# Kernel optimization log

Measured on AMD Instinct MI355X. Metric: run time of the kernel, lower is better.

The kernel has to match this reference:

```python
import jax, jax.numpy as jnp
import numpy as np

N = 50000      # nodes
E = 800000     # edges
P = 3          # pos_dim
F = 64         # feats_dim
M = 32         # m_dim
L = 2          # n_layers
EIN = 2 * F + 1  # edge_input_dim = 129
EPS = 1e-8


def _xavier(key, shape):
    # per-layer stacked xavier-normal weights, shape = (in, out)
    fan_in, fan_out = shape
    std = (2.0 / (fan_in + fan_out)) ** 0.5
    return std * jax.random.normal(key, (L,) + shape, jnp.float32)


def setup_inputs() -> dict:
    key = jax.random.key(0)
    ks = jax.random.split(key, 10)
    x = jax.random.normal(ks[0], (N, P + F), jnp.float32)
    edge_index = jax.random.randint(ks[1], (2, E), 0, N)
    return {
        "x": x,
        "edge_index": edge_index,
        # edge_mlp: Linear(EIN, 2*EIN) -> SiLU -> Linear(2*EIN, M) -> SiLU
        "eW1": _xavier(ks[2], (EIN, 2 * EIN)), "eb1": jnp.zeros((L, 2 * EIN), jnp.float32),
        "eW2": _xavier(ks[3], (2 * EIN, M)),   "eb2": jnp.zeros((L, M), jnp.float32),
        # coors_mlp: Linear(M, 4*M) -> SiLU -> Linear(4*M, 1) -> Tanh
        "cW1": _xavier(ks[4], (M, 4 * M)),     "cb1": jnp.zeros((L, 4 * M), jnp.float32),
        "cW2": _xavier(ks[5], (4 * M, 1)),     "cb2": jnp.zeros((L, 1), jnp.float32),
        # node_mlp: Linear(F+M, 2*F) -> SiLU -> Linear(2*F, F)
        "nW1": _xavier(ks[6], (F + M, 2 * F)), "nb1": jnp.zeros((L, 2 * F), jnp.float32),
        "nW2": _xavier(ks[7], (2 * F, F)),     "nb2": jnp.zeros((L, F), jnp.float32),
        # CoorsNorm learned scale (init 0.01) per layer
        "cscale": jnp.full((L, 1), 0.01, jnp.float32),
    }


def reference(x, edge_index, eW1, eb1, eW2, eb2, cW1, cb1, cW2, cb2,
              nW1, nb1, nW2, nb2, cscale):
    src = edge_index[0]  # x_j (source)
    dst = edge_index[1]  # x_i (target / aggregation index)
    for l in range(L):
        coors, feats = x[:, :P], x[:, P:]
        rel = coors[src] - coors[dst]                       # (E, 3)
        rel_dist = jnp.sum(rel * rel, axis=-1, keepdims=True)  # (E, 1)
        # per-edge message MLP
        e_in = jnp.concatenate([feats[dst], feats[src], rel_dist], axis=-1)  # (E, 129)
        h = jax.nn.silu(e_in @ eW1[l] + eb1[l])             # (E, 258)
        m_ij = jax.nn.silu(h @ eW2[l] + eb2[l])             # (E, 32)
        # coordinate weights: SiLU MLP -> tanh
        cw = jnp.tanh(jax.nn.silu(m_ij @ cW1[l] + cb1[l]) @ cW2[l] + cb2[l])  # (E, 1)
        # CoorsNorm on rel_coors
        norm = jnp.linalg.norm(rel, axis=-1, keepdims=True)
        rel_n = rel / jnp.maximum(norm, EPS) * cscale[l]
        # scatter-aggregate (aggr='add')
        mhat_i = jax.ops.segment_sum(cw * rel_n, dst, num_segments=N)  # (N, 3)
        coors_out = coors + mhat_i
        m_i = jax.ops.segment_sum(m_ij, dst, num_segments=N)           # (N, 32)
        # node update MLP with residual
        n_in = jnp.concatenate([feats, m_i], axis=-1)                  # (N, 96)
        upd = jax.nn.silu(n_in @ nW1[l] + nb1[l]) @ nW2[l] + nb2[l]    # (N, 64)
        x = jnp.concatenate([coors_out, feats + upd], axis=-1)
    return x
```

## Files before the change

kernel.cpp:

```cpp
#include <hip/hip_runtime.h>

#define N_NODES 50000
#define N_EDGES 800000
#define PDIM 3
#define FDIM 64
#define MDIM 32
#define NLAYERS 2
#define EINDIM 129
#define H1 258
#define CH 128
#define NH 128
#define XDIM 67
#define K1P 136
#define H1T 288
#define HSTR 168
#define W1T_K 136
#define MLSTR 40
#define NINS 104
#define NH1S 136
#define NW2K 128

typedef __attribute__((ext_vector_type(8))) short short8;
typedef __attribute__((ext_vector_type(4))) float f32x4;

#define LOG2E 1.4426950408889634f

__device__ __forceinline__ float fsilu(float x) {
  float e = __builtin_amdgcn_exp2f(-x * LOG2E);
  return x * __builtin_amdgcn_rcpf(1.0f + e);
}

__device__ __forceinline__ float ftanh(float x) {
  float xc = fminf(fmaxf(x, -15.0f), 15.0f);
  float E = __builtin_amdgcn_exp2f(2.0f * LOG2E * xc);
  return (E - 1.0f) * __builtin_amdgcn_rcpf(E + 1.0f);
}

__device__ __forceinline__ unsigned short f2bf(float f) {
  union { float f; unsigned u; } v; v.f = f;
  unsigned r = v.u + 0x7FFF + ((v.u >> 16) & 1);
  return (unsigned short)(r >> 16);
}

__device__ __forceinline__ unsigned cvt_pk(float lo, float hi) {
  unsigned r;
  asm("v_cvt_pk_bf16_f32 %0, %1, %2" : "=v"(r) : "v"(lo), "v"(hi));
  return r;
}

__device__ __forceinline__ int xcd_swz(int bid, int nwg) {
  const int nx = 8;
  int q = nwg / nx, r = nwg % nx;
  int xcd = bid % nx, idx = bid / nx;
  return (xcd < r) ? xcd * (q + 1) + idx : r * (q + 1) + (xcd - r) * q + idx;
}

__global__ void count_kernel(const int* __restrict__ ei, int* __restrict__ cnt) {
  int e = blockIdx.x * 256 + threadIdx.x;
  if (e < N_EDGES) atomicAdd(&cnt[ei[N_EDGES + e]], 1);
}

__global__ __launch_bounds__(1024)
void scan_kernel(const int* __restrict__ cnt, int* __restrict__ csr, int* __restrict__ cursor) {
  __shared__ int partial[1024];
  const int tid = threadIdx.x;
  const int CHUNK = 49;
  int base = tid * CHUNK;
  int s = 0;
  for (int i = 0; i < CHUNK; ++i) {
    int idx = base + i;
    if (idx < N_NODES) s += cnt[idx];
  }
  partial[tid] = s;
  __syncthreads();
  for (int off = 1; off < 1024; off <<= 1) {
    int v = (tid >= off) ? partial[tid - off] : 0;
    __syncthreads();
    partial[tid] += v;
    __syncthreads();
  }
  int run = partial[tid] - s;
  for (int i = 0; i < CHUNK; ++i) {
    int idx = base + i;
    if (idx < N_NODES) {
      csr[idx] = run;
      cursor[idx] = run;
      run += cnt[idx];
    }
  }
  if (tid == 1023) csr[N_NODES] = run;
}

__global__ void rank_kernel(const int* __restrict__ ei, int* __restrict__ cursor,
                            int* __restrict__ srcS, int* __restrict__ dstS) {
  int e = blockIdx.x * 256 + threadIdx.x;
  if (e < N_EDGES) {
    int s = ei[e];
    int d = ei[N_EDGES + e];
    int p = atomicAdd(&cursor[d], 1);
    srcS[p] = s;
    dstS[p] = d;
  }
}

__global__ void prep_weights(const float* __restrict__ eW1, const float* __restrict__ eW2,
                             const float* __restrict__ cW1, const float* __restrict__ eb1,
                             const float* __restrict__ nW1, const float* __restrict__ nW2,
                             unsigned short* __restrict__ w1t, unsigned short* __restrict__ w2t,
                             unsigned short* __restrict__ cw1t,
                             unsigned short* __restrict__ nw1t, unsigned short* __restrict__ nw2t,
                             float* __restrict__ b1p, float* __restrict__ wrp) {
  int idx = blockIdx.x * 256 + threadIdx.x;
  const int n1 = NLAYERS * H1T * W1T_K;
  const int n2 = NLAYERS * MDIM * H1T;
  const int n3 = NLAYERS * CH * MDIM;
  const int n4 = NLAYERS * H1T;
  const int n5 = NLAYERS * NH * NINS;
  const int n6 = NLAYERS * FDIM * NW2K;
  if (idx < n1) {
    int k = idx % W1T_K;
    int rest = idx / W1T_K;
    int j = rest % H1T;
    int l = rest / H1T;
    float v = (k < 128 && j < H1) ? eW1[(l * EINDIM + k) * H1 + j] : 0.0f;
    w1t[idx] = f2bf(v);
  } else if (idx < n1 + n2) {
    int t = idx - n1;
    int k = t % H1T;
    int rest = t / H1T;
    int n = rest % MDIM;
    int l = rest / MDIM;
    float v = (k < H1) ? eW2[(l * H1 + k) * MDIM + n] : 0.0f;
    w2t[t] = f2bf(v);
  } else if (idx < n1 + n2 + n3) {
    int t = idx - n1 - n2;
    int k = t % MDIM;
    int rest = t / MDIM;
    int n = rest % CH;
    int l = rest / CH;
    cw1t[t] = f2bf(cW1[(l * MDIM + k) * CH + n]);
  } else if (idx < n1 + n2 + n3 + n4) {
    int t = idx - n1 - n2 - n3;
    int j = t % H1T;
    int l = t / H1T;
    b1p[t] = (j < H1) ? eb1[l * H1 + j] : 0.0f;
  } else if (idx < n1 + n2 + n3 + 2 * n4) {
    int t = idx - n1 - n2 - n3 - n4;
    int j = t % H1T;
    int l = t / H1T;
    wrp[t] = (j < H1) ? eW1[((size_t)l * EINDIM + 128) * H1 + j] : 0.0f;
  } else if (idx < n1 + n2 + n3 + 2 * n4 + n5) {
    int t = idx - n1 - n2 - n3 - 2 * n4;
    int k = t % NINS;
    int rest = t / NINS;
    int j = rest % NH;
    int l = rest / NH;
    float v = (k < FDIM + MDIM) ? nW1[(l * (FDIM + MDIM) + k) * NH + j] : 0.0f;
    nw1t[t] = f2bf(v);
  } else if (idx < n1 + n2 + n3 + 2 * n4 + n5 + n6) {
    int t = idx - n1 - n2 - n3 - 2 * n4 - n5;
    int k = t % NW2K;
    int rest = t / NW2K;
    int j = rest % FDIM;
    int l = rest / FDIM;
    nw2t[t] = f2bf(nW2[(l * NH + k) * FDIM + j]);
  }
}

__global__ void convert_x(const float* __restrict__ X, unsigned short* __restrict__ Xb) {
  int idx = blockIdx.x * 256 + threadIdx.x;
  if (idx >= N_NODES * 8) return;
  int n = idx >> 3, c = idx & 7;
  const float* src = X + n * XDIM + PDIM + c * 8;
  short8 v;
  #pragma unroll
  for (int i = 0; i < 8; ++i) v[i] = (short)f2bf(src[i]);
  *(short8*)&Xb[n * 64 + c * 8] = v;
}

__global__ __launch_bounds__(256, 3)
void edge_mfma_kernel(const float* __restrict__ X,
                      const unsigned short* __restrict__ Xb,
                      const int* __restrict__ srcS, const int* __restrict__ dstS,
                      const unsigned short* __restrict__ w1t,
                      const float* __restrict__ b1p, const float* __restrict__ wrp,
                      const unsigned short* __restrict__ w2t, const float* __restrict__ eb2,
                      const unsigned short* __restrict__ cw1t, const float* __restrict__ cb1,
                      const float* __restrict__ cW2, const float* __restrict__ cb2,
                      const float* __restrict__ cscale,
                      unsigned short* __restrict__ ms, float* __restrict__ mh4,
                      int layer)
{
  __shared__ unsigned short einLds[64 * K1P];
  __shared__ unsigned short hLds[64 * HSTR];
  __shared__ unsigned short ml[64 * MLSTR];
  __shared__ float distLds[64];
  __shared__ float rel3[64 * 3];
  __shared__ int sdS[64], sdD[64];

  const int tid = threadIdx.x;
  const int lane = tid & 63;
  const int wid = tid >> 6;
  const int ln15 = lane & 15;
  const int kg = lane >> 4;
  const int e0 = xcd_swz(blockIdx.x, gridDim.x) * 64;
  const int erow = wid * 16 + ln15;

  if (tid < 64) {
    int s = srcS[e0 + tid];
    int d = dstS[e0 + tid];
    sdS[tid] = s; sdD[tid] = d;
    float rx = X[s * XDIM + 0] - X[d * XDIM + 0];
    float ry = X[s * XDIM + 1] - X[d * XDIM + 1];
    float rz = X[s * XDIM + 2] - X[d * XDIM + 2];
    rel3[tid * 3 + 0] = rx;
    rel3[tid * 3 + 1] = ry;
    rel3[tid * 3 + 2] = rz;
    distLds[tid] = rx * rx + ry * ry + rz * rz;
  }
  __syncthreads();

  #pragma unroll
  for (int it = 0; it < 4; ++it) {
    int idx = tid + it * 256;
    int e = idx >> 4, c = idx & 15;
    int node = (c < 8) ? sdD[e] : sdS[e];
    short8 v = *(const short8*)&Xb[node * 64 + (c & 7) * 8];
    *(short8*)&einLds[e * K1P + c * 8] = v;
  }
  __syncthreads();

  float distE[4];
  #pragma unroll
  for (int et = 0; et < 4; ++et) distE[et] = distLds[et * 16 + ln15];

  const unsigned short* W1T = w1t + layer * H1T * W1T_K;
  const float* B1P = b1p + layer * H1T;
  const float* WRP = wrp + layer * H1T;
  const unsigned short* W2T = w2t + layer * MDIM * H1T;
  const float* B2 = eb2 + layer * MDIM;

  float b20 = B2[ln15], b21 = B2[16 + ln15];
  f32x4 mac0 = {b20, b20, b20, b20};
  f32x4 mac1 = {b21, b21, b21, b21};

  #pragma unroll 1
  for (int half = 0; half < 2; ++half) {
    const int jt0 = half ? 10 : 0;
    const int njt = half ? 8 : 10;
    for (int jl = wid; jl < njt; jl += 4) {
      const int jt = jt0 + jl;
      f32x4 b4 = *(const f32x4*)&B1P[jt * 16 + kg * 4];
      f32x4 w4 = *(const f32x4*)&WRP[jt * 16 + kg * 4];
      short8 a[4];
      #pragma unroll
      for (int ks = 0; ks < 4; ++ks)
        a[ks] = *(const short8*)&W1T[(jt * 16 + ln15) * W1T_K + ks * 32 + kg * 8];
      #pragma unroll
      for (int et = 0; et < 4; ++et) {
        f32x4 acc;
        #pragma unroll
        for (int r = 0; r < 4; ++r) acc[r] = fmaf(distE[et], w4[r], b4[r]);
        #pragma unroll
        for (int ks = 0; ks < 4; ++ks) {
          short8 b = *(const short8*)&einLds[(et * 16 + ln15) * K1P + ks * 32 + kg * 8];
          acc = __builtin_amdgcn_mfma_f32_16x16x32_bf16(a[ks], b, acc, 0, 0, 0);
        }
        uint2 uu;
        uu.x = cvt_pk(fsilu(acc[0]), fsilu(acc[1]));
        uu.y = cvt_pk(fsilu(acc[2]), fsilu(acc[3]));
        *(uint2*)&hLds[(et * 16 + ln15) * HSTR + jl * 16 + kg * 4] = uu;
      }
    }
    __syncthreads();

    const int nks = half ? 4 : 5;
    #pragma unroll
    for (int ksl = 0; ksl < nks; ++ksl) {
      const int kglob = half * 160 + ksl * 32;
      short8 ah = *(const short8*)&hLds[erow * HSTR + ksl * 32 + kg * 8];
      short8 w0 = *(const short8*)&W2T[ln15 * H1T + kglob + kg * 8];
      short8 w1 = *(const short8*)&W2T[(16 + ln15) * H1T + kglob + kg * 8];
      mac0 = __builtin_amdgcn_mfma_f32_16x16x32_bf16(ah, w0, mac0, 0, 0, 0);
      mac1 = __builtin_amdgcn_mfma_f32_16x16x32_bf16(ah, w1, mac1, 0, 0, 0);
    }
    if (half == 0) __syncthreads();
  }

  #pragma unroll
  for (int r = 0; r < 4; ++r) {
    int e = wid * 16 + kg * 4 + r;
    ml[e * MLSTR + ln15] = f2bf(fsilu(mac0[r]));
    ml[e * MLSTR + 16 + ln15] = f2bf(fsilu(mac1[r]));
  }

  const unsigned short* CW1T = cw1t + layer * CH * MDIM;
  const float* CB1 = cb1 + layer * CH;
  const float* CW2v = cW2 + layer * CH;
  short8 am = *(const short8*)&ml[erow * MLSTR + kg * 8];
  float psum[4] = {0.f, 0.f, 0.f, 0.f};
  #pragma unroll
  for (int nt = 0; nt < 8; ++nt) {
    float cb = CB1[nt * 16 + ln15];
    f32x4 cacc = {cb, cb, cb, cb};
    short8 bc = *(const short8*)&CW1T[(nt * 16 + ln15) * MDIM + kg * 8];
    cacc = __builtin_amdgcn_mfma_f32_16x16x32_bf16(am, bc, cacc, 0, 0, 0);
    float w2v = CW2v[nt * 16 + ln15];
    #pragma unroll
    for (int r = 0; r < 4; ++r) psum[r] += fsilu(cacc[r]) * w2v;
  }
  #pragma unroll
  for (int off = 1; off < 16; off <<= 1) {
    #pragma unroll
    for (int r = 0; r < 4; ++r) psum[r] += __shfl_xor(psum[r], off, 64);
  }
  float cwv = 0.0f;
  #pragma unroll
  for (int r = 0; r < 4; ++r) {
    float t = __shfl(psum[r], ((lane & 15) >> 2) * 16, 64);
    if ((lane & 3) == r) cwv = t;
  }

  {
    int e_loc = lane >> 2, seg = lane & 3;
    short8 v = *(const short8*)&ml[(wid * 16 + e_loc) * MLSTR + seg * 8];
    *(short8*)&ms[(size_t)(e0 + wid * 16 + e_loc) * MDIM + seg * 8] = v;
  }
  if (lane < 16) {
    int eg = e0 + erow;
    float cw = ftanh(cwv + cb2[layer]);
    float fac = cw * cscale[layer] / fmaxf(sqrtf(distLds[erow]), 1e-8f);
    *(float4*)&mh4[(size_t)eg * 4] =
        make_float4(fac * rel3[erow * 3 + 0], fac * rel3[erow * 3 + 1],
                    fac * rel3[erow * 3 + 2], 0.0f);
  }
}

__global__ __launch_bounds__(256, 3)
void node_mfma_kernel(const float* __restrict__ Xin,
                      const unsigned short* __restrict__ XbIn,
                      const unsigned short* __restrict__ ms,
                      const float* __restrict__ mh4,
                      const int* __restrict__ csr,
                      const unsigned short* __restrict__ nw1t, const float* __restrict__ nb1,
                      const unsigned short* __restrict__ nw2t, const float* __restrict__ nb2,
                      float* __restrict__ Xout, unsigned short* __restrict__ XbOut,
                      int writeXb, int layer)
{
  __shared__ unsigned short ninLds[64 * NINS];
  __shared__ unsigned short h1Lds[64 * NH1S];
  __shared__ float outLds[64 * 68];
  __shared__ float mhsLds[64][3];
  __shared__ int csrLds[65];

  const int tid = threadIdx.x;
  const int lane = tid & 63;
  const int wid = tid >> 6;
  const int ln15 = lane & 15;
  const int kg = lane >> 4;
  const int n0 = xcd_swz(blockIdx.x, gridDim.x) * 64;

  if (tid < 65) {
    int nn = n0 + tid;
    csrLds[tid] = (nn <= N_NODES) ? csr[nn] : 0;
  }
  #pragma unroll
  for (int it = 0; it < 2; ++it) {
    int idx = tid + it * 256;
    int nl = idx >> 3, c = idx & 7;
    int n = n0 + nl;
    uint4 v = make_uint4(0, 0, 0, 0);
    if (n < N_NODES) v = *(const uint4*)&XbIn[n * 64 + c * 8];
    *(uint4*)&ninLds[nl * NINS + c * 8] = v;
  }
  __syncthreads();

  {
    const int nl = tid >> 2, sub = tid & 3;
    const int n = n0 + nl;
    int off = csrLds[nl], end = csrLds[nl + 1];
    if (n >= N_NODES) { off = 0; end = 0; }
    float s0 = 0, s1 = 0, s2 = 0, s3 = 0, s4 = 0, s5 = 0, s6 = 0, s7 = 0;
    for (int r = off; r < end; ++r) {
      uint4 q = *(const uint4*)&ms[(size_t)r * MDIM + sub * 8];
      union { unsigned u; float f; } t;
      t.u = q.x << 16;         s0 += t.f;
      t.u = q.x & 0xFFFF0000u; s1 += t.f;
      t.u = q.y << 16;         s2 += t.f;
      t.u = q.y & 0xFFFF0000u; s3 += t.f;
      t.u = q.z << 16;         s4 += t.f;
      t.u = q.z & 0xFFFF0000u; s5 += t.f;
      t.u = q.w << 16;         s6 += t.f;
      t.u = q.w & 0xFFFF0000u; s7 += t.f;
    }
    uint4 mo;
    mo.x = cvt_pk(s0, s1);
    mo.y = cvt_pk(s2, s3);
    mo.z = cvt_pk(s4, s5);
    mo.w = cvt_pk(s6, s7);
    *(uint4*)&ninLds[nl * NINS + FDIM + sub * 8] = mo;

    float mx = 0, my = 0, mz = 0;
    for (int r = off + sub; r < end; r += 4) {
      float4 q = *(const float4*)&mh4[(size_t)r * 4];
      mx += q.x; my += q.y; mz += q.z;
    }
    mx += __shfl_xor(mx, 1, 64); mx += __shfl_xor(mx, 2, 64);
    my += __shfl_xor(my, 1, 64); my += __shfl_xor(my, 2, 64);
    mz += __shfl_xor(mz, 1, 64); mz += __shfl_xor(mz, 2, 64);
    if (sub == 0) {
      mhsLds[nl][0] = mx; mhsLds[nl][1] = my; mhsLds[nl][2] = mz;
    }
  }
  __syncthreads();

  const unsigned short* W1 = nw1t + layer * NH * NINS;
  const float* B1 = nb1 + layer * NH;
  for (int jt = wid; jt < 8; jt += 4) {
    f32x4 b4 = *(const f32x4*)&B1[jt * 16 + kg * 4];
    short8 a[3];
    #pragma unroll
    for (int ks = 0; ks < 3; ++ks)
      a[ks] = *(const short8*)&W1[(jt * 16 + ln15) * NINS + ks * 32 + kg * 8];
    #pragma unroll
    for (int et = 0; et < 4; ++et) {
      f32x4 acc = b4;
      #pragma unroll
      for (int ks = 0; ks < 3; ++ks) {
        short8 b = *(const short8*)&ninLds[(et * 16 + ln15) * NINS + ks * 32 + kg * 8];
        acc = __builtin_amdgcn_mfma_f32_16x16x32_bf16(a[ks], b, acc, 0, 0, 0);
      }
      uint2 uu;
      uu.x = cvt_pk(fsilu(acc[0]), fsilu(acc[1]));
      uu.y = cvt_pk(fsilu(acc[2]), fsilu(acc[3]));
      *(uint2*)&h1Lds[(et * 16 + ln15) * NH1S + jt * 16 + kg * 4] = uu;
    }
  }
  __syncthreads();

  const unsigned short* W2 = nw2t + layer * FDIM * NW2K;
  const float* B2 = nb2 + layer * FDIM;
  {
    int jt = wid;
    f32x4 b4 = *(const f32x4*)&B2[jt * 16 + kg * 4];
    short8 a[4];
    #pragma unroll
    for (int ks = 0; ks < 4; ++ks)
      a[ks] = *(const short8*)&W2[(jt * 16 + ln15) * NW2K + ks * 32 + kg * 8];
    #pragma unroll
    for (int et = 0; et < 4; ++et) {
      f32x4 acc = b4;
      #pragma unroll
      for (int ks = 0; ks < 4; ++ks) {
        short8 b = *(const short8*)&h1Lds[(et * 16 + ln15) * NH1S + ks * 32 + kg * 8];
        acc = __builtin_amdgcn_mfma_f32_16x16x32_bf16(a[ks], b, acc, 0, 0, 0);
      }
      *(f32x4*)&outLds[(et * 16 + ln15) * 68 + jt * 16 + kg * 4] = acc;
    }
  }
  __syncthreads();

  #pragma unroll
  for (int it = 0; it < 16; ++it) {
    int idx = tid + it * 256;
    int nl = idx >> 6, c = idx & 63;
    int n = n0 + nl;
    if (n < N_NODES) {
      float v = Xin[n * XDIM + PDIM + c] + outLds[nl * 68 + c];
      Xout[n * XDIM + PDIM + c] = v;
      if (writeXb) XbOut[n * 64 + c] = f2bf(v);
    }
  }
  if (tid < 64) {
    int n = n0 + tid;
    if (n < N_NODES) {
      Xout[n * XDIM + 0] = Xin[n * XDIM + 0] + mhsLds[tid][0];
      Xout[n * XDIM + 1] = Xin[n * XDIM + 1] + mhsLds[tid][1];
      Xout[n * XDIM + 2] = Xin[n * XDIM + 2] + mhsLds[tid][2];
    }
  }
}

extern "C" void kernel_launch(void* const* d_in, const int* in_sizes, int n_in,
                              void* d_out, int out_size, void* d_ws, size_t ws_size,
                              hipStream_t stream) {
  const float* x      = (const float*)d_in[0];
  const int*   ei     = (const int*)d_in[1];
  const float* eW1    = (const float*)d_in[2];
  const float* eb1    = (const float*)d_in[3];
  const float* eW2    = (const float*)d_in[4];
  const float* eb2    = (const float*)d_in[5];
  const float* cW1    = (const float*)d_in[6];
  const float* cb1    = (const float*)d_in[7];
  const float* cW2    = (const float*)d_in[8];
  const float* cb2    = (const float*)d_in[9];
  const float* nW1    = (const float*)d_in[10];
  const float* nb1    = (const float*)d_in[11];
  const float* nW2    = (const float*)d_in[12];
  const float* nb2    = (const float*)d_in[13];
  const float* cscale = (const float*)d_in[14];

  float* ws     = (float*)d_ws;
  float* X1     = ws;
  float* mh4    = X1 + N_NODES * XDIM;
  int*   csr    = (int*)(mh4 + (size_t)N_EDGES * 4);
  int*   cursor = csr + N_NODES + 4;
  int*   cnt    = cursor + N_NODES;
  int*   srcS   = cnt + N_NODES;
  int*   dstS   = srcS + N_EDGES;
  unsigned short* w1t  = (unsigned short*)(dstS + N_EDGES);
  unsigned short* w2t  = w1t + NLAYERS * H1T * W1T_K;
  unsigned short* cw1t = w2t + NLAYERS * MDIM * H1T;
  unsigned short* nw1t = cw1t + NLAYERS * CH * MDIM;
  unsigned short* nw2t = nw1t + NLAYERS * NH * NINS;
  float* b1p = (float*)(nw2t + NLAYERS * FDIM * NW2K);
  float* wrp = b1p + NLAYERS * H1T;
  unsigned short* Xb = (unsigned short*)(wrp + NLAYERS * H1T);
  unsigned short* ms = Xb + (size_t)N_NODES * 64;

  hipMemsetAsync(cnt, 0, N_NODES * sizeof(int), stream);
  count_kernel<<<(N_EDGES + 255) / 256, 256, 0, stream>>>(ei, cnt);
  scan_kernel<<<1, 1024, 0, stream>>>(cnt, csr, cursor);
  rank_kernel<<<(N_EDGES + 255) / 256, 256, 0, stream>>>(ei, cursor, srcS, dstS);
  {
    const int total = NLAYERS * (H1T * W1T_K + MDIM * H1T + CH * MDIM + 2 * H1T
                                 + NH * NINS + FDIM * NW2K);
    prep_weights<<<(total + 255) / 256, 256, 0, stream>>>(
        eW1, eW2, cW1, eb1, nW1, nW2, w1t, w2t, cw1t, nw1t, nw2t, b1p, wrp);
  }
  convert_x<<<(N_NODES * 8 + 255) / 256, 256, 0, stream>>>(x, Xb);

  const int nodeBlocks = (N_NODES + 63) / 64;
  for (int l = 0; l < NLAYERS; ++l) {
    const float* Xin = (l == 0) ? x : X1;
    float* Xout = (l == 0) ? X1 : (float*)d_out;
    edge_mfma_kernel<<<N_EDGES / 64, 256, 0, stream>>>(
        Xin, Xb, srcS, dstS, w1t, b1p, wrp, w2t, eb2, cw1t, cb1, cW2, cb2, cscale,
        ms, mh4, l);
    node_mfma_kernel<<<nodeBlocks, 256, 0, stream>>>(
        Xin, Xb, ms, mh4, csr, nw1t, nb1, nw2t, nb2, Xout, Xb, (l == 0) ? 1 : 0, l);
  }
}
```

Measured before the change: 734.9 us.

## Make edge MLP wave-private: per-wave 32-edge tiles with register-held inputs

Each wave now owns 32 edges and computes all hidden tiles for them. Its gathered feature operands stay in registers instead of being staged through a shared einLds buffer, so the block-wide barriers go away. The first layer is processed in three chunks of 96 hidden units, each feeding the second layer immediately. That shrinks the shared h buffer and allows 4 blocks per CU with 128 edges per block. The trade-offs are that every wave loads all W1 tiles itself rather than splitting them across waves, and register pressure goes up.

```diff
diff --git a/kernel.cpp b/kernel.cpp
--- a/kernel.cpp
+++ b/kernel.cpp
@@ -11,9 +11,8 @@
 #define CH 128
 #define NH 128
 #define XDIM 67
-#define K1P 136
 #define H1T 288
-#define HSTR 168
+#define HSTR3 104
 #define W1T_K 136
 #define MLSTR 40
 #define NINS 104
@@ -178,7 +177,7 @@
   *(short8*)&Xb[n * 64 + c * 8] = v;
 }
 
-__global__ __launch_bounds__(256, 3)
+__global__ __launch_bounds__(256, 4)
 void edge_mfma_kernel(const float* __restrict__ X,
                       const unsigned short* __restrict__ Xb,
                       const int* __restrict__ srcS, const int* __restrict__ dstS,
@@ -191,48 +190,38 @@
                       unsigned short* __restrict__ ms, float* __restrict__ mh4,
                       int layer)
 {
-  __shared__ unsigned short einLds[64 * K1P];
-  __shared__ unsigned short hLds[64 * HSTR];
-  __shared__ unsigned short ml[64 * MLSTR];
-  __shared__ float distLds[64];
-  __shared__ float rel3[64 * 3];
-  __shared__ int sdS[64], sdD[64];
+  __shared__ unsigned short hLds[128 * HSTR3];
+  __shared__ unsigned short ml[128 * MLSTR];
 
   const int tid = threadIdx.x;
   const int lane = tid & 63;
   const int wid = tid >> 6;
   const int ln15 = lane & 15;
   const int kg = lane >> 4;
-  const int e0 = xcd_swz(blockIdx.x, gridDim.x) * 64;
-  const int erow = wid * 16 + ln15;
-
-  if (tid < 64) {
-    int s = srcS[e0 + tid];
-    int d = dstS[e0 + tid];
-    sdS[tid] = s; sdD[tid] = d;
-    float rx = X[s * XDIM + 0] - X[d * XDIM + 0];
-    float ry = X[s * XDIM + 1] - X[d * XDIM + 1];
-    float rz = X[s * XDIM + 2] - X[d * XDIM + 2];
-    rel3[tid * 3 + 0] = rx;
-    rel3[tid * 3 + 1] = ry;
-    rel3[tid * 3 + 2] = rz;
-    distLds[tid] = rx * rx + ry * ry + rz * rz;
-  }
-  __syncthreads();
-
-  #pragma unroll
-  for (int it = 0; it < 4; ++it) {
-    int idx = tid + it * 256;
-    int e = idx >> 4, c = idx & 15;
-    int node = (c < 8) ? sdD[e] : sdS[e];
-    short8 v = *(const short8*)&Xb[node * 64 + (c & 7) * 8];
-    *(short8*)&einLds[e * K1P + c * 8] = v;
-  }
-  __syncthreads();
-
-  float distE[4];
-  #pragma unroll
-  for (int et = 0; et < 4; ++et) distE[et] = distLds[et * 16 + ln15];
+  const int e0 = xcd_swz(blockIdx.x, gridDim.x) * 128;
+  const int ew0 = e0 + wid * 32;
+
+  const int eA = ew0 + ln15;
+  const int eB = ew0 + 16 + ln15;
+  const int sA = srcS[eA], dA = dstS[eA];
+  const int sB = srcS[eB], dB = dstS[eB];
+  float rxA = X[sA * XDIM + 0] - X[dA * XDIM + 0];
+  float ryA = X[sA * XDIM + 1] - X[dA * XDIM + 1];
+  float rzA = X[sA * XDIM + 2] - X[dA * XDIM + 2];
+  float rxB = X[sB * XDIM + 0] - X[dB * XDIM + 0];
+  float ryB = X[sB * XDIM + 1] - X[dB * XDIM + 1];
+  float rzB = X[sB * XDIM + 2] - X[dB * XDIM + 2];
+  const float distA = rxA * rxA + ryA * ryA + rzA * rzA;
+  const float distB = rxB * rxB + ryB * ryB + rzB * rzB;
+
+  short8 einB[2][4];
+  #pragma unroll
+  for (int ks = 0; ks < 4; ++ks) {
+    int nA = (ks < 2) ? dA : sA;
+    int nB = (ks < 2) ? dB : sB;
+    einB[0][ks] = *(const short8*)&Xb[nA * 64 + (ks & 1) * 32 + kg * 8];
+    einB[1][ks] = *(const short8*)&Xb[nB * 64 + (ks & 1) * 32 + kg * 8];
+  }
 
   const unsigned short* W1T = w1t + layer * H1T * W1T_K;
   const float* B1P = b1p + layer * H1T;
@@ -241,14 +230,18 @@
   const float* B2 = eb2 + layer * MDIM;
 
   float b20 = B2[ln15], b21 = B2[16 + ln15];
-  f32x4 mac0 = {b20, b20, b20, b20};
-  f32x4 mac1 = {b21, b21, b21, b21};
+  f32x4 mac[2][2];
+  #pragma unroll
+  for (int et = 0; et < 2; ++et) {
+    mac[et][0] = (f32x4){b20, b20, b20, b20};
+    mac[et][1] = (f32x4){b21, b21, b21, b21};
+  }
 
   #pragma unroll 1
-  for (int half = 0; half < 2; ++half) {
-    const int jt0 = half ? 10 : 0;
-    const int njt = half ? 8 : 10;
-    for (int jl = wid; jl < njt; jl += 4) {
+  for (int chunk = 0; chunk < 3; ++chunk) {
+    const int jt0 = chunk * 6;
+    #pragma unroll 2
+    for (int jl = 0; jl < 6; ++jl) {
       const int jt = jt0 + jl;
       f32x4 b4 = *(const f32x4*)&B1P[jt * 16 + kg * 4];
       f32x4 w4 = *(const f32x4*)&WRP[jt * 16 + kg * 4];
@@ -257,82 +250,97 @@
       for (int ks = 0; ks < 4; ++ks)
         a[ks] = *(const short8*)&W1T[(jt * 16 + ln15) * W1T_K + ks * 32 + kg * 8];
       #pragma unroll
-      for (int et = 0; et < 4; ++et) {
+      for (int et = 0; et < 2; ++et) {
+        const float dv = et ? distB : distA;
         f32x4 acc;
         #pragma unroll
-        for (int r = 0; r < 4; ++r) acc[r] = fmaf(distE[et], w4[r], b4[r]);
+        for (int r = 0; r < 4; ++r) acc[r] = fmaf(dv, w4[r], b4[r]);
         #pragma unroll
-        for (int ks = 0; ks < 4; ++ks) {
-          short8 b = *(const short8*)&einLds[(et * 16 + ln15) * K1P + ks * 32 + kg * 8];
-          acc = __builtin_amdgcn_mfma_f32_16x16x32_bf16(a[ks], b, acc, 0, 0, 0);
-        }
+        for (int ks = 0; ks < 4; ++ks)
+          acc = __builtin_amdgcn_mfma_f32_16x16x32_bf16(a[ks], einB[et][ks], acc, 0, 0, 0);
         uint2 uu;
         uu.x = cvt_pk(fsilu(acc[0]), fsilu(acc[1]));
         uu.y = cvt_pk(fsilu(acc[2]), fsilu(acc[3]));
-        *(uint2*)&hLds[(et * 16 + ln15) * HSTR + jl * 16 + kg * 4] = uu;
+        *(uint2*)&hLds[(wid * 32 + et * 16 + ln15) * HSTR3 + jl * 16 + kg * 4] = uu;
       }
     }
-    __syncthreads();
-
-    const int nks = half ? 4 : 5;
-    #pragma unroll
-    for (int ksl = 0; ksl < nks; ++ksl) {
-      const int kglob = half * 160 + ksl * 32;
-      short8 ah = *(const short8*)&hLds[erow * HSTR + ksl * 32 + kg * 8];
+    #pragma unroll
+    for (int ksl = 0; ksl < 3; ++ksl) {
+      const int kglob = chunk * 96 + ksl * 32;
       short8 w0 = *(const short8*)&W2T[ln15 * H1T + kglob + kg * 8];
       short8 w1 = *(const short8*)&W2T[(16 + ln15) * H1T + kglob + kg * 8];
-      mac0 = __builtin_amdgcn_mfma_f32_16x16x32_bf16(ah, w0, mac0, 0, 0, 0);
-      mac1 = __builtin_amdgcn_mfma_f32_16x16x32_bf16(ah, w1, mac1, 0, 0, 0);
-    }
-    if (half == 0) __syncthreads();
-  }
-
-  #pragma unroll
-  for (int r = 0; r < 4; ++r) {
-    int e = wid * 16 + kg * 4 + r;
-    ml[e * MLSTR + ln15] = f2bf(fsilu(mac0[r]));
-    ml[e * MLSTR + 16 + ln15] = f2bf(fsilu(mac1[r]));
+      #pragma unroll
+      for (int et = 0; et < 2; ++et) {
+        short8 ah = *(const short8*)&hLds[(wid * 32 + et * 16 + ln15) * HSTR3 + ksl * 32 + kg * 8];
+        mac[et][0] = __builtin_amdgcn_mfma_f32_16x16x32_bf16(ah, w0, mac[et][0], 0, 0, 0);
+        mac[et][1] = __builtin_amdgcn_mfma_f32_16x16x32_bf16(ah, w1, mac[et][1], 0, 0, 0);
+      }
+    }
+  }
+
+  #pragma unroll
+  for (int et = 0; et < 2; ++et) {
+    #pragma unroll
+    for (int r = 0; r < 4; ++r) {
+      int eg = wid * 32 + et * 16 + kg * 4 + r;
+      ml[eg * MLSTR + ln15] = f2bf(fsilu(mac[et][0][r]));
+      ml[eg * MLSTR + 16 + ln15] = f2bf(fsilu(mac[et][1][r]));
+    }
   }
 
   const unsigned short* CW1T = cw1t + layer * CH * MDIM;
   const float* CB1 = cb1 + layer * CH;
   const float* CW2v = cW2 + layer * CH;
-  short8 am = *(const short8*)&ml[erow * MLSTR + kg * 8];
-  float psum[4] = {0.f, 0.f, 0.f, 0.f};
+  short8 amA = *(const short8*)&ml[(wid * 32 + ln15) * MLSTR + kg * 8];
+  short8 amB = *(const short8*)&ml[(wid * 32 + 16 + ln15) * MLSTR + kg * 8];
+  float psA[4] = {0.f, 0.f, 0.f, 0.f};
+  float psB[4] = {0.f, 0.f, 0.f, 0.f};
   #pragma unroll
   for (int nt = 0; nt < 8; ++nt) {
     float cb = CB1[nt * 16 + ln15];
-    f32x4 cacc = {cb, cb, cb, cb};
+    float w2v = CW2v[nt * 16 + ln15];
     short8 bc = *(const short8*)&CW1T[(nt * 16 + ln15) * MDIM + kg * 8];
-    cacc = __builtin_amdgcn_mfma_f32_16x16x32_bf16(am, bc, cacc, 0, 0, 0);
-    float w2v = CW2v[nt * 16 + ln15];
-    #pragma unroll
-    for (int r = 0; r < 4; ++r) psum[r] += fsilu(cacc[r]) * w2v;
+    f32x4 cA = {cb, cb, cb, cb};
+    f32x4 cB = {cb, cb, cb, cb};
+    cA = __builtin_amdgcn_mfma_f32_16x16x32_bf16(amA, bc, cA, 0, 0, 0);
+    cB = __builtin_amdgcn_mfma_f32_16x16x32_bf16(amB, bc, cB, 0, 0, 0);
+    #pragma unroll
+    for (int r = 0; r < 4; ++r) {
+      psA[r] += fsilu(cA[r]) * w2v;
+      psB[r] += fsilu(cB[r]) * w2v;
+    }
   }
   #pragma unroll
   for (int off = 1; off < 16; off <<= 1) {
     #pragma unroll
-    for (int r = 0; r < 4; ++r) psum[r] += __shfl_xor(psum[r], off, 64);
-  }
-  float cwv = 0.0f;
+    for (int r = 0; r < 4; ++r) {
+      psA[r] += __shfl_xor(psA[r], off, 64);
+      psB[r] += __shfl_xor(psB[r], off, 64);
+    }
+  }
+  float cwvA = 0.0f, cwvB = 0.0f;
   #pragma unroll
   for (int r = 0; r < 4; ++r) {
-    float t = __shfl(psum[r], ((lane & 15) >> 2) * 16, 64);
-    if ((lane & 3) == r) cwv = t;
-  }
-
-  {
-    int e_loc = lane >> 2, seg = lane & 3;
-    short8 v = *(const short8*)&ml[(wid * 16 + e_loc) * MLSTR + seg * 8];
-    *(short8*)&ms[(size_t)(e0 + wid * 16 + e_loc) * MDIM + seg * 8] = v;
-  }
-  if (lane < 16) {
-    int eg = e0 + erow;
+    float tA = __shfl(psA[r], ((lane & 15) >> 2) * 16, 64);
+    float tB = __shfl(psB[r], ((lane & 15) >> 2) * 16, 64);
+    if ((lane & 3) == r) { cwvA = tA; cwvB = tB; }
+  }
+
+  #pragma unroll
+  for (int it = 0; it < 2; ++it) {
+    int idx = lane + it * 64;
+    int el = idx >> 2, seg = idx & 3;
+    short8 v = *(const short8*)&ml[(wid * 32 + el) * MLSTR + seg * 8];
+    *(short8*)&ms[(size_t)(ew0 + el) * MDIM + seg * 8] = v;
+  }
+  if (lane < 32) {
+    const int hi = lane >> 4;
+    float cwv = hi ? cwvB : cwvA;
+    float dv = hi ? distB : distA;
+    float rx = hi ? rxB : rxA, ry = hi ? ryB : ryA, rz = hi ? rzB : rzA;
     float cw = ftanh(cwv + cb2[layer]);
-    float fac = cw * cscale[layer] / fmaxf(sqrtf(distLds[erow]), 1e-8f);
-    *(float4*)&mh4[(size_t)eg * 4] =
-        make_float4(fac * rel3[erow * 3 + 0], fac * rel3[erow * 3 + 1],
-                    fac * rel3[erow * 3 + 2], 0.0f);
+    float fac = cw * cscale[layer] / fmaxf(sqrtf(dv), 1e-8f);
+    *(float4*)&mh4[(size_t)(ew0 + lane) * 4] = make_float4(fac * rx, fac * ry, fac * rz, 0.0f);
   }
 }
 
@@ -534,7 +542,7 @@
   for (int l = 0; l < NLAYERS; ++l) {
     const float* Xin = (l == 0) ? x : X1;
     float* Xout = (l == 0) ? X1 : (float*)d_out;
-    edge_mfma_kernel<<<N_EDGES / 64, 256, 0, stream>>>(
+    edge_mfma_kernel<<<N_EDGES / 128, 256, 0, stream>>>(
         Xin, Xb, srcS, dstS, w1t, b1p, wrp, w2t, eb2, cw1t, cb1, cW2, cb2, cscale,
         ms, mh4, l);
     node_mfma_kernel<<<nodeBlocks, 256, 0, stream>>>(
```

Result: faster. 692.5 us (-5.8%).
